# Kernel tuning notes

Hardware: AMD Instinct MI355X
Metric: run time of the kernel (lower is better)

Reference implementation:

```python
import jax, jax.numpy as jnp
import numpy as np

N_NODES = 40000
N_EDGES = 640000
IN_FEATS = 128
HID = 64
# layer widths per GCN.__init__: in->h->2h->2h->h->h->h->1
DIMS = [IN_FEATS, HID, 2 * HID, 2 * HID, HID, HID, HID, 1]


def setup_inputs() -> dict:
    key = jax.random.key(0)
    ks = jax.random.split(key, 3 + 2 * 7)
    inp = {
        "in_feat": jax.random.normal(ks[0], (N_NODES, IN_FEATS), dtype=jnp.float32),
        "src": jax.random.randint(ks[1], (N_EDGES,), 0, N_NODES, dtype=jnp.int32),
        "dst": jax.random.randint(ks[2], (N_EDGES,), 0, N_NODES, dtype=jnp.int32),
    }
    # DGL GraphConv params: weight [in, out] (glorot), bias [out] (zeros; use small randn for a nontrivial baseline)
    for i in range(7):
        din, dout = DIMS[i], DIMS[i + 1]
        scale = jnp.sqrt(6.0 / (din + dout)).astype(jnp.float32)
        inp[f"W{i+1}"] = jax.random.uniform(ks[3 + 2 * i], (din, dout), jnp.float32, -scale, scale)
        inp[f"b{i+1}"] = 0.01 * jax.random.normal(ks[4 + 2 * i], (dout,), dtype=jnp.float32)
    return inp


def _graph_conv(x, W, b, src, dst, out_norm, in_norm, n_nodes):
    # DGL GraphConv, norm='both', allow_zero_in_degree=True:
    #   h = D_in^{-1/2} * A^T * (D_out^{-1/2} * x) @ W + b
    x = x * out_norm[:, None]
    if x.shape[1] > W.shape[1]:
        # mult W first to shrink message dim (mirrors DGL's heuristic; math-equivalent)
        x = x @ W
        h = jax.ops.segment_sum(x[src], dst, num_segments=n_nodes)
    else:
        h = jax.ops.segment_sum(x[src], dst, num_segments=n_nodes)
        h = h @ W
    return h * in_norm[:, None] + b


def reference(in_feat, src, dst, W1, b1, W2, b2, W3, b3, W4, b4, W5, b5, W6, b6, W7, b7):
    n = in_feat.shape[0]
    ones = jnp.ones((src.shape[0],), dtype=jnp.float32)
    out_deg = jax.ops.segment_sum(ones, src, num_segments=n)
    in_deg = jax.ops.segment_sum(ones, dst, num_segments=n)
    out_norm = jnp.where(out_deg > 0, jax.lax.rsqrt(jnp.maximum(out_deg, 1.0)), 0.0)
    in_norm = jnp.where(in_deg > 0, jax.lax.rsqrt(jnp.maximum(in_deg, 1.0)), 0.0)

    params = [(W1, b1), (W2, b2), (W3, b3), (W4, b4), (W5, b5), (W6, b6), (W7, b7)]
    h = in_feat
    for i, (W, b) in enumerate(params):
        h = _graph_conv(h, W, b, src, dst, out_norm, in_norm, n)
        if i < 6:
            h = jax.nn.relu(h)
    return h  # [N, 1]
```

## Files before the change

### kernel.cpp

```cpp
#include <hip/hip_runtime.h>
#include <hip/hip_bf16.h>


#define IN_F 128
#define NSLICE 60
#define SHB 13
#define NSHARD 5

typedef __attribute__((ext_vector_type(8))) short short8v;
typedef __attribute__((ext_vector_type(4))) float f32x4;
typedef __attribute__((ext_vector_type(8))) _Float16 half8v;

static __device__ __forceinline__ unsigned short f2bf(float x) {
    unsigned u = __builtin_bit_cast(unsigned, x);
    unsigned r = (u + 0x7FFFu + ((u >> 16) & 1u)) >> 16;
    return (unsigned short)r;
}
static __device__ __forceinline__ float bf2f(unsigned short h) {
    unsigned u = ((unsigned)h) << 16;
    return __builtin_bit_cast(float, u);
}


__global__ __launch_bounds__(256) void hist2_kernel(const int* __restrict__ src,
                                                    const int* __restrict__ dst,
                                                    int* __restrict__ scratch, int E) {
    constexpr int SH = 1 << SHB;
    __shared__ int h[SH];
    const int t = threadIdx.x;
    const int b = blockIdx.x;
    const int s = blockIdx.y;
    const int z = blockIdx.z;
    const int* idx = z ? dst : src;
    for (int i = t; i < SH; i += 256) h[i] = 0;
    __syncthreads();
    const int per = (E + NSLICE - 1) / NSLICE;
    const int lo = b * per;
    const int hiE = min(lo + per, E);
    const int base = s << SHB;
    for (int e = lo + t; e < hiE; e += 256) {
        unsigned a = (unsigned)(idx[e] - base);
        if (a < (unsigned)SH) atomicAdd(&h[a], 1);
    }
    __syncthreads();
    int* so = scratch + ((size_t)((z * NSHARD + s) * NSLICE + b) << SHB);
    for (int i = t; i < SH; i += 256) so[i] = h[i];
}

__global__ void hist_reduce_kernel(const int* __restrict__ scratch,
                                   int* __restrict__ in_deg,
                                   float* __restrict__ out_nrm,
                                   float* __restrict__ in_nrm, int N) {
    constexpr int SH = 1 << SHB;
    int n = blockIdx.x * blockDim.x + threadIdx.x;
    if (n >= N) return;
    int s = n >> SHB;
    int i = n & (SH - 1);
    int od = 0, idg = 0;
    for (int b = 0; b < NSLICE; ++b) {
        od  += scratch[((size_t)((0 * NSHARD + s) * NSLICE + b) << SHB) + i];
        idg += scratch[((size_t)((1 * NSHARD + s) * NSLICE + b) << SHB) + i];
    }
    in_deg[n] = idg;
    out_nrm[n] = od  > 0 ? rsqrtf((float)od)  : 0.f;
    in_nrm[n]  = idg > 0 ? rsqrtf((float)idg) : 0.f;
}


__global__ __launch_bounds__(256) void scan_blk_kernel(const int* __restrict__ deg,
                                                       int* __restrict__ blockSums, int N) {
    __shared__ int ws[4];
    const int t = threadIdx.x;
    const int base = blockIdx.x * 1024 + t * 4;
    int4 v = make_int4(0, 0, 0, 0);
    if (base + 3 < N) v = *reinterpret_cast<const int4*>(&deg[base]);
    else if (base < N) {
        v.x = deg[base];
        if (base + 1 < N) v.y = deg[base + 1];
        if (base + 2 < N) v.z = deg[base + 2];
    }
    int s = v.x + v.y + v.z + v.w;
#pragma unroll
    for (int off = 32; off > 0; off >>= 1) s += __shfl_down(s, off);
    if ((t & 63) == 0) ws[t >> 6] = s;
    __syncthreads();
    if (t == 0) blockSums[blockIdx.x] = ws[0] + ws[1] + ws[2] + ws[3];
}

__global__ __launch_bounds__(64) void scan_top_kernel(const int* __restrict__ blockSums,
                                                      int* __restrict__ blockOffs,
                                                      int* __restrict__ row_off, int NB, int N) {
    const int t = threadIdx.x;
    int orig = (t < NB) ? blockSums[t] : 0;
    int v = orig;
#pragma unroll
    for (int off = 1; off < 64; off <<= 1) {
        int u = __shfl_up(v, off);
        if (t >= off) v += u;
    }
    if (t < NB) blockOffs[t] = v - orig;
    if (t == 63) row_off[N] = v;
}

__global__ __launch_bounds__(256) void scan_fill_kernel(const int* __restrict__ deg,
                                                        const int* __restrict__ blockOffs,
                                                        int* __restrict__ row_off, int N) {
    __shared__ int wtot[4];
    const int t = threadIdx.x;
    const int lane = t & 63;
    const int wid = t >> 6;
    const int base = blockIdx.x * 1024 + t * 4;
    int4 v = make_int4(0, 0, 0, 0);
    if (base + 3 < N) v = *reinterpret_cast<const int4*>(&deg[base]);
    else if (base < N) {
        v.x = deg[base];
        if (base + 1 < N) v.y = deg[base + 1];
        if (base + 2 < N) v.z = deg[base + 2];
    }
    const int s = v.x + v.y + v.z + v.w;
    int incl = s;
#pragma unroll
    for (int off = 1; off < 64; off <<= 1) {
        int u = __shfl_up(incl, off);
        if (lane >= off) incl += u;
    }
    if (lane == 63) wtot[wid] = incl;
    __syncthreads();
    int pre = blockOffs[blockIdx.x] + incl - s;
    for (int i = 0; i < wid; ++i) pre += wtot[i];
    if (base < N) {
        int run = pre;
        row_off[base] = run; run += v.x;
        if (base + 1 < N) { row_off[base + 1] = run; run += v.y; }
        if (base + 2 < N) { row_off[base + 2] = run; run += v.z; }
        if (base + 3 < N) { row_off[base + 3] = run; }
    }
}

__global__ void slice_base_kernel(int* __restrict__ scratch,
                                  const int* __restrict__ row_off, int N) {
    constexpr int SH = 1 << SHB;
    int n = blockIdx.x * blockDim.x + threadIdx.x;
    if (n >= N) return;
    int s = n >> SHB;
    int i = n & (SH - 1);
    int run = row_off[n];
    for (int b = 0; b < NSLICE; ++b) {
        size_t off = ((size_t)((NSHARD + s) * NSLICE + b) << SHB) + i;
        int c = scratch[off];
        scratch[off] = run;
        run += c;
    }
}

__global__ __launch_bounds__(256) void fill2_kernel(const int* __restrict__ src,
                                                    const int* __restrict__ dst,
                                                    const int* __restrict__ scratch,
                                                    int* __restrict__ csr, int E) {
    constexpr int SH = 1 << SHB;
    __shared__ int cur[SH];
    const int t = threadIdx.x;
    const int b = blockIdx.x;
    const int s = blockIdx.y;
    const int* base = scratch + ((size_t)((NSHARD + s) * NSLICE + b) << SHB);
    for (int i = t; i < SH; i += 256) cur[i] = base[i];
    __syncthreads();
    const int per = (E + NSLICE - 1) / NSLICE;
    const int lo = b * per;
    const int hiE = min(lo + per, E);
    const int nb = s << SHB;
    for (int e = lo + t; e < hiE; e += 256) {
        unsigned a = (unsigned)(dst[e] - nb);
        if (a < (unsigned)SH) {
            int pos = atomicAdd(&cur[a], 1);
            csr[pos] = src[e];
        }
    }
}


struct WDesc { const float* w; unsigned short* th; unsigned short* tl; int K; int N; };
struct WPack { WDesc d[6]; };

__global__ __launch_bounds__(256) void split_w_kernel(WPack p) {
    WDesc d = p.d[blockIdx.x];
    int i = blockIdx.y * 256 + threadIdx.x;
    if (i >= d.K * d.N) return;
    int k = i / d.N, n = i - k * d.N;
    float v = d.w[i];
    unsigned short h = f2bf(v);
    d.th[(size_t)n * d.K + k] = h;
    d.tl[(size_t)n * d.K + k] = f2bf(v - bf2f(h));
}


template<int K, int NOUT>
__global__ __launch_bounds__(256) void gemm_mfma_f32(
    const float* __restrict__ X,
    const unsigned short* __restrict__ Bh, const unsigned short* __restrict__ Bl,
    const float* __restrict__ pre, _Float16* __restrict__ Y16, int M) {
    constexpr int NT = NOUT / 16;
    const int lane = threadIdx.x & 63;
    const int wv = threadIdx.x >> 6;
    const int r0 = blockIdx.x * 64 + wv * 16;
    const int arow = r0 + (lane & 15);
    const int kg = (lane >> 4) * 8;
    const float sc = pre[arow];

    f32x4 acc[NT];
#pragma unroll
    for (int n = 0; n < NT; ++n) acc[n] = (f32x4){0.f, 0.f, 0.f, 0.f};

    for (int kk = 0; kk < K; kk += 32) {
        const float* ap = &X[(size_t)arow * K + kk + kg];
        float4 v0 = *reinterpret_cast<const float4*>(ap);
        float4 v1 = *reinterpret_cast<const float4*>(ap + 4);
        float a[8] = {v0.x, v0.y, v0.z, v0.w, v1.x, v1.y, v1.z, v1.w};
        short8v a_h, a_l;
#pragma unroll
        for (int j = 0; j < 8; ++j) {
            float f = a[j] * sc;
            unsigned short hh = f2bf(f);
            a_h[j] = (short)hh;
            a_l[j] = (short)f2bf(f - bf2f(hh));
        }
#pragma unroll
        for (int n = 0; n < NT; ++n) {
            int col = n * 16 + (lane & 15);
            short8v b_h = *reinterpret_cast<const short8v*>(Bh + (size_t)col * K + kk + kg);
            short8v b_l = *reinterpret_cast<const short8v*>(Bl + (size_t)col * K + kk + kg);
            acc[n] = __builtin_amdgcn_mfma_f32_16x16x32_bf16(a_h, b_h, acc[n], 0, 0, 0);
            acc[n] = __builtin_amdgcn_mfma_f32_16x16x32_bf16(a_h, b_l, acc[n], 0, 0, 0);
            acc[n] = __builtin_amdgcn_mfma_f32_16x16x32_bf16(a_l, b_h, acc[n], 0, 0, 0);
        }
    }
    const int c0 = lane & 15;
    const int rr = r0 + (lane >> 4) * 4;
#pragma unroll
    for (int n = 0; n < NT; ++n) {
        const int col = n * 16 + c0;
#pragma unroll
        for (int j = 0; j < 4; ++j)
            Y16[(size_t)(rr + j) * NOUT + col] = (_Float16)acc[n][j];
    }
}


template<int K, int NOUT, bool EPI>
__global__ __launch_bounds__(256) void gemm_h16(
    const _Float16* __restrict__ X,
    const unsigned short* __restrict__ Bh, const unsigned short* __restrict__ Bl,
    const float* __restrict__ r_nrm, const float* __restrict__ s_nrm,
    const float* __restrict__ bias, _Float16* __restrict__ Y16, int M) {
    constexpr int NT = NOUT / 16;
    const int lane = threadIdx.x & 63;
    const int wv = threadIdx.x >> 6;
    const int r0 = blockIdx.x * 64 + wv * 16;
    const int arow = r0 + (lane & 15);
    const int kg = (lane >> 4) * 8;

    f32x4 acc[NT];
#pragma unroll
    for (int n = 0; n < NT; ++n) acc[n] = (f32x4){0.f, 0.f, 0.f, 0.f};

    for (int kk = 0; kk < K; kk += 32) {
        half8v av = *reinterpret_cast<const half8v*>(&X[(size_t)arow * K + kk + kg]);
        short8v a_h, a_l;
#pragma unroll
        for (int j = 0; j < 8; ++j) {
            float f = (float)av[j];
            unsigned short hh = f2bf(f);
            a_h[j] = (short)hh;
            a_l[j] = (short)f2bf(f - bf2f(hh));
        }
#pragma unroll
        for (int n = 0; n < NT; ++n) {
            int col = n * 16 + (lane & 15);
            short8v b_h = *reinterpret_cast<const short8v*>(Bh + (size_t)col * K + kk + kg);
            short8v b_l = *reinterpret_cast<const short8v*>(Bl + (size_t)col * K + kk + kg);
            acc[n] = __builtin_amdgcn_mfma_f32_16x16x32_bf16(a_h, b_h, acc[n], 0, 0, 0);
            acc[n] = __builtin_amdgcn_mfma_f32_16x16x32_bf16(a_h, b_l, acc[n], 0, 0, 0);
            acc[n] = __builtin_amdgcn_mfma_f32_16x16x32_bf16(a_l, b_h, acc[n], 0, 0, 0);
        }
    }
    const int c0 = lane & 15;
    const int rr = r0 + (lane >> 4) * 4;
#pragma unroll
    for (int n = 0; n < NT; ++n) {
        const int col = n * 16 + c0;
        const float bcol = EPI ? bias[col] : 0.f;
#pragma unroll
        for (int j = 0; j < 4; ++j) {
            const int row = rr + j;
            float y = acc[n][j];
            if (EPI) {
                y = fmaf(y, r_nrm[row], bcol);
                y = fmaxf(y, 0.f);
                y *= s_nrm[row];
            }
            Y16[(size_t)row * NOUT + col] = (_Float16)y;
        }
    }
}


template<int F, bool EPI>
__global__ __launch_bounds__(256) void agg_h16(
    const _Float16* __restrict__ X, const int* __restrict__ csr,
    const int* __restrict__ row_off, const float* __restrict__ r_nrm,
    const float* __restrict__ s_nrm, const float* __restrict__ bias,
    _Float16* __restrict__ Y16, int N) {
    constexpr int LPE = F / 8;
    constexpr int EPW = 64 / LPE;
    const int lane = threadIdx.x & 63;
    const int node = blockIdx.x * (blockDim.x >> 6) + (threadIdx.x >> 6);
    if (node >= N) return;
    const int g = lane / LPE;
    const int c = lane % LPE;
    const int lo = row_off[node];
    const int hi = row_off[node + 1];
    float acc[8], acc2[8];
#pragma unroll
    for (int j = 0; j < 8; ++j) { acc[j] = 0.f; acc2[j] = 0.f; }
    int e = lo + g;
    for (; e + EPW < hi; e += 2 * EPW) {
        int s0 = csr[e];
        int s1 = csr[e + EPW];
        half8v x0 = *reinterpret_cast<const half8v*>(&X[(size_t)s0 * F + c * 8]);
        half8v x1 = *reinterpret_cast<const half8v*>(&X[(size_t)s1 * F + c * 8]);
#pragma unroll
        for (int j = 0; j < 8; ++j) { acc[j] += (float)x0[j]; acc2[j] += (float)x1[j]; }
    }
    if (e < hi) {
        int s0 = csr[e];
        half8v x0 = *reinterpret_cast<const half8v*>(&X[(size_t)s0 * F + c * 8]);
#pragma unroll
        for (int j = 0; j < 8; ++j) acc[j] += (float)x0[j];
    }
#pragma unroll
    for (int j = 0; j < 8; ++j) acc[j] += acc2[j];
#pragma unroll
    for (int m = LPE; m < 64; m <<= 1) {
#pragma unroll
        for (int j = 0; j < 8; ++j) acc[j] += __shfl_xor(acc[j], m);
    }
    if (lane < LPE) {
        half8v o;
        if (EPI) {
            float rn = r_nrm[node];
            float sn = s_nrm[node];
#pragma unroll
            for (int j = 0; j < 8; ++j) {
                float y = fmaf(acc[j], rn, bias[lane * 8 + j]);
                o[j] = (_Float16)(fmaxf(y, 0.f) * sn);
            }
        } else {
#pragma unroll
            for (int j = 0; j < 8; ++j) o[j] = (_Float16)acc[j];
        }
        *reinterpret_cast<half8v*>(&Y16[(size_t)node * F + lane * 8]) = o;
    }
}


__global__ __launch_bounds__(256) void gemv64_kernel(const _Float16* __restrict__ X,
                                                     const float* __restrict__ W,
                                                     float* __restrict__ Y, int M) {
    const int lane = threadIdx.x & 63;
    const int m = blockIdx.x * (blockDim.x >> 6) + (threadIdx.x >> 6);
    if (m >= M) return;
    float v = (float)X[(size_t)m * 64 + lane] * W[lane];
#pragma unroll
    for (int off = 32; off > 0; off >>= 1) v += __shfl_down(v, off);
    if (lane == 0) Y[m] = v;
}

__global__ __launch_bounds__(256) void agg1_kernel(const float* __restrict__ T,
                                                   const int* __restrict__ csr,
                                                   const int* __restrict__ row_off,
                                                   const float* __restrict__ r_nrm,
                                                   const float* __restrict__ bias,
                                                   float* __restrict__ Y, int N) {
    const int node = blockIdx.x * 16 + (threadIdx.x >> 4);
    const int l = threadIdx.x & 15;
    if (node >= N) return;
    const int lo = row_off[node];
    const int hi = row_off[node + 1];
    float acc = 0.f;
    for (int e = lo + l; e < hi; e += 16) acc += T[csr[e]];
#pragma unroll
    for (int m = 8; m >= 1; m >>= 1) acc += __shfl_xor(acc, m);
    if (l == 0) Y[node] = fmaf(acc, r_nrm[node], bias[0]);
}


extern "C" void kernel_launch(void* const* d_in, const int* in_sizes, int n_in,
                              void* d_out, int out_size, void* d_ws, size_t ws_size,
                              hipStream_t stream) {
    const float* in_feat = (const float*)d_in[0];
    const int* src = (const int*)d_in[1];
    const int* dst = (const int*)d_in[2];
    const float* W1 = (const float*)d_in[3];  const float* B1 = (const float*)d_in[4];
    const float* W2 = (const float*)d_in[5];  const float* B2 = (const float*)d_in[6];
    const float* W3 = (const float*)d_in[7];  const float* B3 = (const float*)d_in[8];
    const float* W4 = (const float*)d_in[9];  const float* B4 = (const float*)d_in[10];
    const float* W5 = (const float*)d_in[11]; const float* B5 = (const float*)d_in[12];
    const float* W6 = (const float*)d_in[13]; const float* B6 = (const float*)d_in[14];
    const float* W7 = (const float*)d_in[15]; const float* B7 = (const float*)d_in[16];

    const int N = in_sizes[0] / IN_F;
    const int E = in_sizes[1];
    float* out = (float*)d_out;

    char* w = (char*)d_ws;
    auto alloc = [&](size_t bytes) { char* p = w; w += (bytes + 255) & ~(size_t)255; return p; };
    int* csr      = (int*)alloc((size_t)E * 4);
    int* row_off  = (int*)alloc((size_t)(N + 1) * 4);
    int* in_deg   = (int*)alloc((size_t)N * 4);
    int* blockSums= (int*)alloc(64 * 4);
    int* blockOffs= (int*)alloc(64 * 4);
    float* out_nrm= (float*)alloc((size_t)N * 4);
    float* in_nrm = (float*)alloc((size_t)N * 4);
    float* t7     = (float*)alloc((size_t)N * 4);
    const int dims[8] = {128, 64, 128, 128, 64, 64, 64, 1};
    unsigned short* wth[6]; unsigned short* wtl[6];
    for (int i = 0; i < 6; ++i) {
        size_t kn = (size_t)dims[i] * dims[i + 1];
        wth[i] = (unsigned short*)alloc(kn * 2);
        wtl[i] = (unsigned short*)alloc(kn * 2);
    }
    _Float16* h0 = (_Float16*)alloc((size_t)N * 128 * 2);
    _Float16* h1 = (_Float16*)alloc((size_t)N * 128 * 2);
    int* scratch = (int*)h0;
    (void)ws_size; (void)n_in; (void)out_size;

    const int TB = 256;
    const int NB = (N + 1023) / 1024;

    WPack wp;
    const float* Ws[6] = {W1, W2, W3, W4, W5, W6};
    for (int i = 0; i < 6; ++i) wp.d[i] = {Ws[i], wth[i], wtl[i], dims[i], dims[i + 1]};
    split_w_kernel<<<dim3(6, 64), TB, 0, stream>>>(wp);

    hist2_kernel<<<dim3(NSLICE, NSHARD, 2), TB, 0, stream>>>(src, dst, scratch, E);
    hist_reduce_kernel<<<(N + TB - 1) / TB, TB, 0, stream>>>(
        scratch, in_deg, out_nrm, in_nrm, N);
    scan_blk_kernel<<<NB, TB, 0, stream>>>(in_deg, blockSums, N);
    scan_top_kernel<<<1, 64, 0, stream>>>(blockSums, blockOffs, row_off, NB, N);
    scan_fill_kernel<<<NB, TB, 0, stream>>>(in_deg, blockOffs, row_off, N);
    slice_base_kernel<<<(N + TB - 1) / TB, TB, 0, stream>>>(scratch, row_off, N);
    fill2_kernel<<<dim3(NSLICE, NSHARD), TB, 0, stream>>>(src, dst, scratch, csr, E);

    const int gridN4 = (N + 3) / 4;
    const int MB = (N + 63) / 64;

    gemm_mfma_f32<128, 64><<<MB, TB, 0, stream>>>(in_feat, wth[0], wtl[0], out_nrm, h0, N);
    agg_h16<64, true><<<gridN4, TB, 0, stream>>>(h0, csr, row_off, in_nrm, out_nrm, B1, h1, N);

    agg_h16<64, false><<<gridN4, TB, 0, stream>>>(h1, csr, row_off, nullptr, nullptr, nullptr, h0, N);
    gemm_h16<64, 128, true><<<MB, TB, 0, stream>>>(h0, wth[1], wtl[1], in_nrm, out_nrm, B2, h1, N);

    agg_h16<128, false><<<gridN4, TB, 0, stream>>>(h1, csr, row_off, nullptr, nullptr, nullptr, h0, N);
    gemm_h16<128, 128, true><<<MB, TB, 0, stream>>>(h0, wth[2], wtl[2], in_nrm, out_nrm, B3, h1, N);

    gemm_h16<128, 64, false><<<MB, TB, 0, stream>>>(h1, wth[3], wtl[3], nullptr, nullptr, nullptr, h0, N);
    agg_h16<64, true><<<gridN4, TB, 0, stream>>>(h0, csr, row_off, in_nrm, out_nrm, B4, h1, N);

    agg_h16<64, false><<<gridN4, TB, 0, stream>>>(h1, csr, row_off, nullptr, nullptr, nullptr, h0, N);
    gemm_h16<64, 64, true><<<MB, TB, 0, stream>>>(h0, wth[4], wtl[4], in_nrm, out_nrm, B5, h1, N);

    agg_h16<64, false><<<gridN4, TB, 0, stream>>>(h1, csr, row_off, nullptr, nullptr, nullptr, h0, N);
    gemm_h16<64, 64, true><<<MB, TB, 0, stream>>>(h0, wth[5], wtl[5], in_nrm, out_nrm, B6, h1, N);

    gemv64_kernel<<<gridN4, TB, 0, stream>>>(h1, W7, t7, N);
    agg1_kernel<<<(N + 15) / 16, TB, 0, stream>>>(t7, csr, row_off, in_nrm, B7, out, N);
}
```

Measured before the change: 306.0 us.

## Fuse aggregation with small GEMM per node and merge degree reduce with scan

Adds a fused kernel that gathers 64-wide neighbor features for each node, then applies the layer weight (stored as fp16) in registers via shuffles, plus bias, ReLU and norm. For the last hidden layer it also folds in the final W7 dot product. This replaces separate agg, GEMM and gemv launches for layers 2, 5 and 6 and drops the intermediate round-trips through global memory. The degree histogram reduce is merged with the block-sum scan stage, using vector loads over padded node arrays. The per-node scalar FMA loop and fp16 weights stand in for split-bf16 MFMA, which adds ALU work and may change precision slightly.

```diff
diff --git a/kernel.cpp b/kernel.cpp
--- a/kernel.cpp
+++ b/kernel.cpp
@@ -47,44 +47,43 @@
     for (int i = t; i < SH; i += 256) so[i] = h[i];
 }
 
-__global__ void hist_reduce_kernel(const int* __restrict__ scratch,
-                                   int* __restrict__ in_deg,
-                                   float* __restrict__ out_nrm,
-                                   float* __restrict__ in_nrm, int N) {
+__global__ __launch_bounds__(256) void hist_reduce_blk(
+    const int* __restrict__ scratch, int* __restrict__ in_deg,
+    float* __restrict__ out_nrm, float* __restrict__ in_nrm,
+    int* __restrict__ blockSums) {
     constexpr int SH = 1 << SHB;
-    int n = blockIdx.x * blockDim.x + threadIdx.x;
-    if (n >= N) return;
-    int s = n >> SHB;
-    int i = n & (SH - 1);
-    int od = 0, idg = 0;
-    for (int b = 0; b < NSLICE; ++b) {
-        od  += scratch[((size_t)((0 * NSHARD + s) * NSLICE + b) << SHB) + i];
-        idg += scratch[((size_t)((1 * NSHARD + s) * NSLICE + b) << SHB) + i];
-    }
-    in_deg[n] = idg;
-    out_nrm[n] = od  > 0 ? rsqrtf((float)od)  : 0.f;
-    in_nrm[n]  = idg > 0 ? rsqrtf((float)idg) : 0.f;
-}
-
-
-__global__ __launch_bounds__(256) void scan_blk_kernel(const int* __restrict__ deg,
-                                                       int* __restrict__ blockSums, int N) {
-    __shared__ int ws[4];
+    __shared__ int ws4[4];
     const int t = threadIdx.x;
     const int base = blockIdx.x * 1024 + t * 4;
-    int4 v = make_int4(0, 0, 0, 0);
-    if (base + 3 < N) v = *reinterpret_cast<const int4*>(&deg[base]);
-    else if (base < N) {
-        v.x = deg[base];
-        if (base + 1 < N) v.y = deg[base + 1];
-        if (base + 2 < N) v.z = deg[base + 2];
-    }
-    int s = v.x + v.y + v.z + v.w;
-#pragma unroll
-    for (int off = 32; off > 0; off >>= 1) s += __shfl_down(s, off);
-    if ((t & 63) == 0) ws[t >> 6] = s;
+    const int s = base >> SHB;
+    const int i = base & (SH - 1);
+    int od[4] = {0, 0, 0, 0}, id[4] = {0, 0, 0, 0};
+    const int* po = scratch + (((size_t)s * NSLICE) << SHB) + i;
+    const int* pi = scratch + (((size_t)(NSHARD + s) * NSLICE) << SHB) + i;
+    for (int b = 0; b < NSLICE; ++b) {
+        int4 o4 = *reinterpret_cast<const int4*>(po + ((size_t)b << SHB));
+        int4 i4 = *reinterpret_cast<const int4*>(pi + ((size_t)b << SHB));
+        od[0] += o4.x; od[1] += o4.y; od[2] += o4.z; od[3] += o4.w;
+        id[0] += i4.x; id[1] += i4.y; id[2] += i4.z; id[3] += i4.w;
+    }
+    *reinterpret_cast<int4*>(&in_deg[base]) = make_int4(id[0], id[1], id[2], id[3]);
+    float4 onf, inf;
+    onf.x = od[0] > 0 ? rsqrtf((float)od[0]) : 0.f;
+    onf.y = od[1] > 0 ? rsqrtf((float)od[1]) : 0.f;
+    onf.z = od[2] > 0 ? rsqrtf((float)od[2]) : 0.f;
+    onf.w = od[3] > 0 ? rsqrtf((float)od[3]) : 0.f;
+    inf.x = id[0] > 0 ? rsqrtf((float)id[0]) : 0.f;
+    inf.y = id[1] > 0 ? rsqrtf((float)id[1]) : 0.f;
+    inf.z = id[2] > 0 ? rsqrtf((float)id[2]) : 0.f;
+    inf.w = id[3] > 0 ? rsqrtf((float)id[3]) : 0.f;
+    *reinterpret_cast<float4*>(&out_nrm[base]) = onf;
+    *reinterpret_cast<float4*>(&in_nrm[base]) = inf;
+    int ssum = id[0] + id[1] + id[2] + id[3];
+#pragma unroll
+    for (int off = 32; off > 0; off >>= 1) ssum += __shfl_down(ssum, off);
+    if ((t & 63) == 0) ws4[t >> 6] = ssum;
     __syncthreads();
-    if (t == 0) blockSums[blockIdx.x] = ws[0] + ws[1] + ws[2] + ws[3];
+    if (t == 0) blockSums[blockIdx.x] = ws4[0] + ws4[1] + ws4[2] + ws4[3];
 }
 
 __global__ __launch_bounds__(64) void scan_top_kernel(const int* __restrict__ blockSums,
@@ -179,7 +178,7 @@
 }
 
 
-struct WDesc { const float* w; unsigned short* th; unsigned short* tl; int K; int N; };
+struct WDesc { const float* w; unsigned short* th; unsigned short* tl; _Float16* t16; int K; int N; };
 struct WPack { WDesc d[6]; };
 
 __global__ __launch_bounds__(256) void split_w_kernel(WPack p) {
@@ -191,6 +190,7 @@
     unsigned short h = f2bf(v);
     d.th[(size_t)n * d.K + k] = h;
     d.tl[(size_t)n * d.K + k] = f2bf(v - bf2f(h));
+    if (d.t16) d.t16[(size_t)n * d.K + k] = (_Float16)v;
 }
 
 
@@ -363,17 +363,80 @@
 }
 
 
-__global__ __launch_bounds__(256) void gemv64_kernel(const _Float16* __restrict__ X,
-                                                     const float* __restrict__ W,
-                                                     float* __restrict__ Y, int M) {
+template<int NOUT, bool LAST>
+__global__ __launch_bounds__(256) void fused_agv(
+    const _Float16* __restrict__ X, const int* __restrict__ csr,
+    const int* __restrict__ row_off, const _Float16* __restrict__ Wt,
+    const float* __restrict__ r_nrm, const float* __restrict__ s_nrm,
+    const float* __restrict__ bias, const float* __restrict__ W7,
+    _Float16* __restrict__ Y16, float* __restrict__ T7, int N) {
     const int lane = threadIdx.x & 63;
-    const int m = blockIdx.x * (blockDim.x >> 6) + (threadIdx.x >> 6);
-    if (m >= M) return;
-    float v = (float)X[(size_t)m * 64 + lane] * W[lane];
-#pragma unroll
-    for (int off = 32; off > 0; off >>= 1) v += __shfl_down(v, off);
-    if (lane == 0) Y[m] = v;
-}
+    const int node = blockIdx.x * 4 + (threadIdx.x >> 6);
+    if (node >= N) return;
+    const int g = lane >> 3;
+    const int c = lane & 7;
+    const int lo = row_off[node];
+    const int hi = row_off[node + 1];
+    float acc[8], acc2[8];
+#pragma unroll
+    for (int j = 0; j < 8; ++j) { acc[j] = 0.f; acc2[j] = 0.f; }
+    int e = lo + g;
+    for (; e + 8 < hi; e += 16) {
+        int s0 = csr[e];
+        int s1 = csr[e + 8];
+        half8v x0 = *reinterpret_cast<const half8v*>(&X[(size_t)s0 * 64 + c * 8]);
+        half8v x1 = *reinterpret_cast<const half8v*>(&X[(size_t)s1 * 64 + c * 8]);
+#pragma unroll
+        for (int j = 0; j < 8; ++j) { acc[j] += (float)x0[j]; acc2[j] += (float)x1[j]; }
+    }
+    if (e < hi) {
+        int s0 = csr[e];
+        half8v x0 = *reinterpret_cast<const half8v*>(&X[(size_t)s0 * 64 + c * 8]);
+#pragma unroll
+        for (int j = 0; j < 8; ++j) acc[j] += (float)x0[j];
+    }
+#pragma unroll
+    for (int j = 0; j < 8; ++j) acc[j] += acc2[j];
+#pragma unroll
+    for (int m = 8; m < 64; m <<= 1) {
+#pragma unroll
+        for (int j = 0; j < 8; ++j) acc[j] += __shfl_xor(acc[j], m);
+    }
+
+    half8v w0[8];
+#pragma unroll
+    for (int q = 0; q < 8; ++q)
+        w0[q] = *reinterpret_cast<const half8v*>(&Wt[(size_t)lane * 64 + q * 8]);
+    half8v w1[8];
+    if (NOUT == 128) {
+#pragma unroll
+        for (int q = 0; q < 8; ++q)
+            w1[q] = *reinterpret_cast<const half8v*>(&Wt[(size_t)(lane + 64) * 64 + q * 8]);
+    }
+    float o0 = 0.f, o1 = 0.f;
+#pragma unroll
+    for (int k = 0; k < 64; ++k) {
+        float tk = __shfl(acc[k & 7], k >> 3);
+        o0 = fmaf(tk, (float)w0[k >> 3][k & 7], o0);
+        if (NOUT == 128) o1 = fmaf(tk, (float)w1[k >> 3][k & 7], o1);
+    }
+    const float rn = r_nrm[node];
+    const float sn = s_nrm[node];
+    float y0 = fmaxf(fmaf(o0, rn, bias[lane]), 0.f) * sn;
+    if (LAST) {
+        float p = y0 * W7[lane];
+#pragma unroll
+        for (int m = 32; m >= 1; m >>= 1) p += __shfl_xor(p, m);
+        if (lane == 0) T7[node] = p;
+    } else {
+        Y16[(size_t)node * NOUT + lane] = (_Float16)y0;
+        if (NOUT == 128) {
+            float y1 = fmaxf(fmaf(o1, rn, bias[lane + 64]), 0.f) * sn;
+            Y16[(size_t)node * NOUT + 64 + lane] = (_Float16)y1;
+        }
+    }
+}
+
 
 __global__ __launch_bounds__(256) void agg1_kernel(const float* __restrict__ T,
                                                    const int* __restrict__ csr,
@@ -410,17 +473,18 @@
 
     const int N = in_sizes[0] / IN_F;
     const int E = in_sizes[1];
+    const int N2 = NSHARD << SHB;
     float* out = (float*)d_out;
 
     char* w = (char*)d_ws;
     auto alloc = [&](size_t bytes) { char* p = w; w += (bytes + 255) & ~(size_t)255; return p; };
     int* csr      = (int*)alloc((size_t)E * 4);
     int* row_off  = (int*)alloc((size_t)(N + 1) * 4);
-    int* in_deg   = (int*)alloc((size_t)N * 4);
+    int* in_deg   = (int*)alloc((size_t)N2 * 4);
     int* blockSums= (int*)alloc(64 * 4);
     int* blockOffs= (int*)alloc(64 * 4);
-    float* out_nrm= (float*)alloc((size_t)N * 4);
-    float* in_nrm = (float*)alloc((size_t)N * 4);
+    float* out_nrm= (float*)alloc((size_t)N2 * 4);
+    float* in_nrm = (float*)alloc((size_t)N2 * 4);
     float* t7     = (float*)alloc((size_t)N * 4);
     const int dims[8] = {128, 64, 128, 128, 64, 64, 64, 1};
     unsigned short* wth[6]; unsigned short* wtl[6];
@@ -429,23 +493,25 @@
         wth[i] = (unsigned short*)alloc(kn * 2);
         wtl[i] = (unsigned short*)alloc(kn * 2);
     }
+    _Float16* w2t16 = (_Float16*)alloc((size_t)64 * 128 * 2);
+    _Float16* w5t16 = (_Float16*)alloc((size_t)64 * 64 * 2);
+    _Float16* w6t16 = (_Float16*)alloc((size_t)64 * 64 * 2);
     _Float16* h0 = (_Float16*)alloc((size_t)N * 128 * 2);
     _Float16* h1 = (_Float16*)alloc((size_t)N * 128 * 2);
     int* scratch = (int*)h0;
     (void)ws_size; (void)n_in; (void)out_size;
 
     const int TB = 256;
-    const int NB = (N + 1023) / 1024;
+    const int NB = N2 / 1024;
 
     WPack wp;
     const float* Ws[6] = {W1, W2, W3, W4, W5, W6};
-    for (int i = 0; i < 6; ++i) wp.d[i] = {Ws[i], wth[i], wtl[i], dims[i], dims[i + 1]};
+    _Float16* t16s[6] = {nullptr, w2t16, nullptr, nullptr, w5t16, w6t16};
+    for (int i = 0; i < 6; ++i) wp.d[i] = {Ws[i], wth[i], wtl[i], t16s[i], dims[i], dims[i + 1]};
     split_w_kernel<<<dim3(6, 64), TB, 0, stream>>>(wp);
 
     hist2_kernel<<<dim3(NSLICE, NSHARD, 2), TB, 0, stream>>>(src, dst, scratch, E);
-    hist_reduce_kernel<<<(N + TB - 1) / TB, TB, 0, stream>>>(
-        scratch, in_deg, out_nrm, in_nrm, N);
-    scan_blk_kernel<<<NB, TB, 0, stream>>>(in_deg, blockSums, N);
+    hist_reduce_blk<<<NB, TB, 0, stream>>>(scratch, in_deg, out_nrm, in_nrm, blockSums);
     scan_top_kernel<<<1, 64, 0, stream>>>(blockSums, blockOffs, row_off, NB, N);
     scan_fill_kernel<<<NB, TB, 0, stream>>>(in_deg, blockOffs, row_off, N);
     slice_base_kernel<<<(N + TB - 1) / TB, TB, 0, stream>>>(scratch, row_off, N);
@@ -457,21 +523,20 @@
     gemm_mfma_f32<128, 64><<<MB, TB, 0, stream>>>(in_feat, wth[0], wtl[0], out_nrm, h0, N);
     agg_h16<64, true><<<gridN4, TB, 0, stream>>>(h0, csr, row_off, in_nrm, out_nrm, B1, h1, N);
 
-    agg_h16<64, false><<<gridN4, TB, 0, stream>>>(h1, csr, row_off, nullptr, nullptr, nullptr, h0, N);
-    gemm_h16<64, 128, true><<<MB, TB, 0, stream>>>(h0, wth[1], wtl[1], in_nrm, out_nrm, B2, h1, N);
-
-    agg_h16<128, false><<<gridN4, TB, 0, stream>>>(h1, csr, row_off, nullptr, nullptr, nullptr, h0, N);
-    gemm_h16<128, 128, true><<<MB, TB, 0, stream>>>(h0, wth[2], wtl[2], in_nrm, out_nrm, B3, h1, N);
-
-    gemm_h16<128, 64, false><<<MB, TB, 0, stream>>>(h1, wth[3], wtl[3], nullptr, nullptr, nullptr, h0, N);
-    agg_h16<64, true><<<gridN4, TB, 0, stream>>>(h0, csr, row_off, in_nrm, out_nrm, B4, h1, N);
-
-    agg_h16<64, false><<<gridN4, TB, 0, stream>>>(h1, csr, row_off, nullptr, nullptr, nullptr, h0, N);
-    gemm_h16<64, 64, true><<<MB, TB, 0, stream>>>(h0, wth[4], wtl[4], in_nrm, out_nrm, B5, h1, N);
-
-    agg_h16<64, false><<<gridN4, TB, 0, stream>>>(h1, csr, row_off, nullptr, nullptr, nullptr, h0, N);
-    gemm_h16<64, 64, true><<<MB, TB, 0, stream>>>(h0, wth[5], wtl[5], in_nrm, out_nrm, B6, h1, N);
-
-    gemv64_kernel<<<gridN4, TB, 0, stream>>>(h1, W7, t7, N);
+    fused_agv<128, false><<<gridN4, TB, 0, stream>>>(
+        h1, csr, row_off, w2t16, in_nrm, out_nrm, B2, nullptr, h0, nullptr, N);
+
+    agg_h16<128, false><<<gridN4, TB, 0, stream>>>(h0, csr, row_off, nullptr, nullptr, nullptr, h1, N);
+    gemm_h16<128, 128, true><<<MB, TB, 0, stream>>>(h1, wth[2], wtl[2], in_nrm, out_nrm, B3, h0, N);
+
+    gemm_h16<128, 64, false><<<MB, TB, 0, stream>>>(h0, wth[3], wtl[3], nullptr, nullptr, nullptr, h1, N);
+    agg_h16<64, true><<<gridN4, TB, 0, stream>>>(h1, csr, row_off, in_nrm, out_nrm, B4, h0, N);
+
+    fused_agv<64, false><<<gridN4, TB, 0, stream>>>(
+        h0, csr, row_off, w5t16, in_nrm, out_nrm, B5, nullptr, h1, nullptr, N);
+
+    fused_agv<64, true><<<gridN4, TB, 0, stream>>>(
+        h1, csr, row_off, w6t16, in_nrm, out_nrm, B6, W7, nullptr, t7, N);
+
     agg1_kernel<<<(N + 15) / 16, TB, 0, stream>>>(t7, csr, row_off, in_nrm, B7, out, N);
 }
```

Measured after the change: 378.8 us. +23.8%, slower.
